# Kernel tuning notes

Measured on AMD Instinct MI355X. Metric: run time of the kernel, lower is better.

The kernel has to match this reference:

```python
import jax, jax.numpy as jnp
import numpy as np

M, K, N, R = 8192, 4096, 4096, 32
GROUP = 64  # nunchaku W4A4 quantization group size
QMAX = 7.0  # int4 symmetric


def setup_inputs() -> dict:
    key = jax.random.key(0)
    ks = jax.random.split(key, 6)
    x = jax.random.normal(ks[0], (M, K), dtype=jnp.float32)
    w_res = jax.random.normal(ks[1], (N, K), dtype=jnp.float32) * 0.02
    lora_down = jax.random.normal(ks[2], (K, R), dtype=jnp.float32) * 0.02
    lora_up = jax.random.normal(ks[3], (N, R), dtype=jnp.float32) * 0.02
    smooth = 0.5 + jax.random.uniform(ks[4], (K,), dtype=jnp.float32)  # positive 1/s factors
    b = jax.random.normal(ks[5], (N,), dtype=jnp.float32)
    return {"x": x, "w_res": w_res, "lora_down": lora_down, "lora_up": lora_up, "smooth": smooth, "b": b}


def _fake_quant_int4(t, group):
    # symmetric int4 fake-quant with per-group absmax scales along last dim
    shp = t.shape
    tg = t.reshape(shp[:-1] + (shp[-1] // group, group))
    scale = jnp.maximum(jnp.max(jnp.abs(tg), axis=-1, keepdims=True) / QMAX, 1e-8)
    q = jnp.clip(jnp.round(tg / scale), -8.0, 7.0) * scale
    return q.reshape(shp)


def reference(x, w_res, lora_down, lora_up, smooth, b):
    # smoothed activation (smooth = 1/s applied by kernel before quantization)
    xs = x * smooth[None, :]                       # [M, K]
    xq = _fake_quant_int4(xs, GROUP)               # per-token per-group int4
    wq = _fake_quant_int4(w_res, GROUP)            # per-outchannel per-group int4
    # W4A4 GEMM on dequantized values + fused low-rank LoRA correction + bias
    main = jnp.einsum('mk,nk->mn', xq, wq)         # [M, N]
    lora = jnp.einsum('mr,nr->mn', xs @ lora_down, lora_up)
    return main + lora + b[None, :]
```

## Files before the change

kernel.cpp:

```cpp
#include <hip/hip_runtime.h>
#include <hip/hip_bf16.h>
#include <stdint.h>

#define M_DIM 8192
#define N_DIM 4096
#define K_DIM 4096
#define R_DIM 32
#define KPAD  4160
#define NT    65
#define QMAXF 7.0f

using bf16_t = __hip_bfloat16;
typedef __attribute__((ext_vector_type(4))) float f32x4;
typedef __attribute__((ext_vector_type(8))) short bf16x8;

__device__ __forceinline__ void stage16(const void* g, void* l) {
#if defined(__has_builtin) && __has_builtin(__builtin_amdgcn_global_load_lds)
  __builtin_amdgcn_global_load_lds(
      (const __attribute__((address_space(1))) unsigned int*)g,
      (__attribute__((address_space(3))) unsigned int*)l, 16, 0, 0);
#else
  *(uint4*)l = *(const uint4*)g;
#endif
}

__global__ __launch_bounds__(256) void prep_kernel(
    const float* __restrict__ x, const float* __restrict__ smooth,
    const float* __restrict__ w, const float* __restrict__ lora_up,
    const float* __restrict__ ld,
    bf16_t* __restrict__ Ap, bf16_t* __restrict__ Bp,
    bf16_t* __restrict__ ldT) {
  const int bid = blockIdx.x;
  const int tid = threadIdx.x;

  if (bid < M_DIM) {
    const int row = bid;
    const int k0  = tid * 16;
    const float* xr = x + (size_t)row * K_DIM + k0;
    const float* sr = smooth + k0;

    float v[16];
#pragma unroll
    for (int i = 0; i < 4; ++i) {
      float4 xv = *(const float4*)(xr + i * 4);
      float4 sv = *(const float4*)(sr + i * 4);
      v[i*4+0] = xv.x * sv.x; v[i*4+1] = xv.y * sv.y;
      v[i*4+2] = xv.z * sv.z; v[i*4+3] = xv.w * sv.w;
    }
    float am = 0.f;
#pragma unroll
    for (int i = 0; i < 16; ++i) am = fmaxf(am, fabsf(v[i]));
    am = fmaxf(am, __shfl_xor(am, 1));
    am = fmaxf(am, __shfl_xor(am, 2));
    const float scale = fmaxf(am / QMAXF, 1e-8f);

    alignas(16) bf16_t o[16];
#pragma unroll
    for (int i = 0; i < 16; ++i) {
      float q = rintf(v[i] / scale);
      q = fminf(fmaxf(q, -8.f), 7.f);
      o[i] = __float2bfloat16(q * scale);
    }
    bf16_t* dst = Ap + (size_t)row * KPAD + k0;
    ((uint4*)dst)[0] = ((uint4*)o)[0];
    ((uint4*)dst)[1] = ((uint4*)o)[1];
    if (tid < 32) Ap[(size_t)row * KPAD + 4128 + tid] = __float2bfloat16(0.f);

  } else if (bid < M_DIM + N_DIM) {
    const int row = bid - M_DIM;
    const int k0  = tid * 16;
    const float* wr = w + (size_t)row * K_DIM + k0;

    float v[16];
#pragma unroll
    for (int i = 0; i < 4; ++i) {
      float4 wv = *(const float4*)(wr + i * 4);
      v[i*4+0] = wv.x; v[i*4+1] = wv.y; v[i*4+2] = wv.z; v[i*4+3] = wv.w;
    }
    float am = 0.f;
#pragma unroll
    for (int i = 0; i < 16; ++i) am = fmaxf(am, fabsf(v[i]));
    am = fmaxf(am, __shfl_xor(am, 1));
    am = fmaxf(am, __shfl_xor(am, 2));
    const float scale = fmaxf(am / QMAXF, 1e-8f);

    alignas(16) bf16_t o[16];
#pragma unroll
    for (int i = 0; i < 16; ++i) {
      float q = rintf(v[i] / scale);
      q = fminf(fmaxf(q, -8.f), 7.f);
      o[i] = __float2bfloat16(q * scale);
    }
    bf16_t* dst = Bp + (size_t)row * KPAD + k0;
    ((uint4*)dst)[0] = ((uint4*)o)[0];
    ((uint4*)dst)[1] = ((uint4*)o)[1];
    if (tid < 32) {
      Bp[(size_t)row * KPAD + 4096 + tid] = __float2bfloat16(lora_up[row * R_DIM + tid]);
    } else if (tid < 64) {
      Bp[(size_t)row * KPAD + 4096 + tid] = __float2bfloat16(0.f);
    }

  } else {
    const int k = (bid - M_DIM - N_DIM) * 256 + tid;
    float v[R_DIM];
#pragma unroll
    for (int i = 0; i < R_DIM / 4; ++i) {
      float4 a = *(const float4*)(ld + (size_t)k * R_DIM + i * 4);
      v[i*4+0] = a.x; v[i*4+1] = a.y; v[i*4+2] = a.z; v[i*4+3] = a.w;
    }
#pragma unroll
    for (int r = 0; r < R_DIM; ++r)
      ldT[(size_t)r * K_DIM + k] = __float2bfloat16(v[r]);
  }
}

__global__ __launch_bounds__(256) void lora_mfma_kernel(
    const float* __restrict__ x, const float* __restrict__ smooth,
    const bf16_t* __restrict__ ldT, bf16_t* __restrict__ Ap) {
  const int tid  = threadIdx.x;
  const int w    = tid >> 6;
  const int lane = tid & 63;
  const int m0   = blockIdx.x * 32;

  const int mrow = m0 + (w >> 1) * 16 + (lane & 15);
  const int ncol = (w & 1) * 16 + (lane & 15);
  const float* xr = x + (size_t)mrow * K_DIM;
  const bf16_t* br = ldT + (size_t)ncol * K_DIM;

  f32x4 acc = {0.f, 0.f, 0.f, 0.f};
  union { bf16_t h[8]; bf16x8 v; } au;

  for (int k = 0; k < K_DIM; k += 32) {
    const int kf = k + (lane >> 4) * 8;
    float4 x0 = *(const float4*)(xr + kf);
    float4 x1 = *(const float4*)(xr + kf + 4);
    float4 s0 = *(const float4*)(smooth + kf);
    float4 s1 = *(const float4*)(smooth + kf + 4);
    au.h[0] = __float2bfloat16(x0.x * s0.x);
    au.h[1] = __float2bfloat16(x0.y * s0.y);
    au.h[2] = __float2bfloat16(x0.z * s0.z);
    au.h[3] = __float2bfloat16(x0.w * s0.w);
    au.h[4] = __float2bfloat16(x1.x * s1.x);
    au.h[5] = __float2bfloat16(x1.y * s1.y);
    au.h[6] = __float2bfloat16(x1.z * s1.z);
    au.h[7] = __float2bfloat16(x1.w * s1.w);
    bf16x8 bv = *(const bf16x8*)(br + kf);
    acc = __builtin_amdgcn_mfma_f32_16x16x32_bf16(au.v, bv, acc, 0, 0, 0);
  }

  const int orow = m0 + (w >> 1) * 16 + (lane >> 4) * 4;
  const int ocol = 4096 + ncol;
#pragma unroll
  for (int q = 0; q < 4; ++q)
    Ap[(size_t)(orow + q) * KPAD + ocol] = __float2bfloat16(acc[q]);
}

__global__ __launch_bounds__(512, 2) void gemm_kernel(
    const bf16_t* __restrict__ A, const bf16_t* __restrict__ B,
    const float* __restrict__ bias, float* __restrict__ C) {
  extern __shared__ __align__(16) bf16_t lds[];

  const int wg  = blockIdx.x;
  const int swz = (wg & 7) * 64 + (wg >> 3);
  const int bn  = swz & 15;
  const int bm  = swz >> 4;

  const int tid  = threadIdx.x;
  const int lane = tid & 63;
  const int wid  = tid >> 6;
  const int wm   = wid >> 2;
  const int wn   = wid & 3;

  const int lr = lane & 15;
  const int lg = lane >> 4;
  const int l7 = lane & 7;
  const int gk0 = ((0 + lg) ^ l7) * 8;
  const int gk1 = ((4 + lg) ^ l7) * 8;

  const int sr   = tid >> 3;
  const int sl   = tid & 7;
  const int gcol = (sl ^ (sr & 7)) * 8;
  const bf16_t* Abase = A + (size_t)(bm * 256 + ((sr >> 5) & 1) * 128 + (sr & 31)) * KPAD + gcol;
  const bf16_t* Bbase = B + (size_t)(bn * 256 + sr) * KPAD + gcol;
  bf16_t* ldsb = lds;

#define STAGE_A(buf, h, kt) do {                                               \
    stage16(Abase + (size_t)((h) * 2 + 0) * 32 * KPAD + (kt) * 64,             \
            ldsb + (buf) * 32768 + (h) * 8192 + 0 * 4096 + tid * 8);           \
    stage16(Abase + (size_t)((h) * 2 + 1) * 32 * KPAD + (kt) * 64,             \
            ldsb + (buf) * 32768 + (h) * 8192 + 1 * 4096 + tid * 8);           \
  } while (0)
#define STAGE_B(buf, h, kt) do {                                               \
    stage16(Bbase + (size_t)((h) * 128 + 0) * KPAD + (kt) * 64,                \
            ldsb + (buf) * 32768 + 16384 + (h) * 8192 + 0 * 4096 + tid * 8);   \
    stage16(Bbase + (size_t)((h) * 128 + 64) * KPAD + (kt) * 64,               \
            ldsb + (buf) * 32768 + 16384 + (h) * 8192 + 1 * 4096 + tid * 8);   \
  } while (0)

  f32x4  acc[8][4] = {};
  bf16x8 aA[2][2];
  bf16x8 aB[2][2];
  bf16x8 bF[4][2];

#define LOAD_A(DST, q, cb) do {                                                \
    const bf16_t* pa_ = ldsb + (cb) * 32768 + ((q) * 64 + wm * 32 + lr) * 64;  \
    DST[0][0] = *(const bf16x8*)(pa_ + gk0);                                   \
    DST[0][1] = *(const bf16x8*)(pa_ + gk1);                                   \
    DST[1][0] = *(const bf16x8*)(pa_ + 1024 + gk0);                            \
    DST[1][1] = *(const bf16x8*)(pa_ + 1024 + gk1);                            \
  } while (0)
#define LOAD_BN(nbuf) do {                                                     \
    _Pragma("unroll")                                                          \
    for (int j = 0; j < 4; ++j) {                                              \
      const bf16_t* pb_ = ldsb + (nbuf) * 32768 + 16384 + (wn * 64 + j * 16 + lr) * 64; \
      bF[j][0] = *(const bf16x8*)(pb_ + gk0);                                  \
      bF[j][1] = *(const bf16x8*)(pb_ + gk1);                                  \
    }                                                                          \
  } while (0)
#define MFMA_Q(q, AARR) do {                                                   \
    _Pragma("unroll")                                                          \
    for (int i = 0; i < 2; ++i)                                                \
      _Pragma("unroll")                                                        \
      for (int j = 0; j < 4; ++j) {                                            \
        acc[(q)*2+i][j] = __builtin_amdgcn_mfma_f32_16x16x32_bf16(             \
            AARR[i][0], bF[j][0], acc[(q)*2+i][j], 0, 0, 0);                   \
        acc[(q)*2+i][j] = __builtin_amdgcn_mfma_f32_16x16x32_bf16(             \
            AARR[i][1], bF[j][1], acc[(q)*2+i][j], 0, 0, 0);                   \
      }                                                                        \
  } while (0)

#define KTILE(u, cur) do {                                                     \
                                                             \
    if ((u) + 1 < NT) STAGE_A((cur) ^ 1, 1, (u) + 1);                          \
    __builtin_amdgcn_s_barrier();                                              \
    asm volatile("s_waitcnt lgkmcnt(0)" ::: "memory");                         \
    __builtin_amdgcn_sched_barrier(0);                                         \
    LOAD_A(aB, 1, cur);                                                        \
    __builtin_amdgcn_sched_barrier(0);                                         \
    __builtin_amdgcn_s_setprio(1);                                             \
    MFMA_Q(0, aA);                                                             \
    __builtin_amdgcn_s_setprio(0);                                             \
    __builtin_amdgcn_s_barrier();                                              \
                                                             \
    if ((u) + 2 < NT) STAGE_B(cur, 0, (u) + 2);                                \
    __builtin_amdgcn_s_barrier();                                              \
    asm volatile("s_waitcnt lgkmcnt(0)" ::: "memory");                         \
    __builtin_amdgcn_sched_barrier(0);                                         \
    LOAD_A(aA, 2, cur);                                                        \
    __builtin_amdgcn_sched_barrier(0);                                         \
    __builtin_amdgcn_s_setprio(1);                                             \
    MFMA_Q(1, aB);                                                             \
    __builtin_amdgcn_s_setprio(0);                                             \
    __builtin_amdgcn_s_barrier();                                              \
                                                             \
    if ((u) + 2 < NT) STAGE_B(cur, 1, (u) + 2);                                \
    __builtin_amdgcn_s_barrier();                                              \
    asm volatile("s_waitcnt lgkmcnt(0)" ::: "memory");                         \
    __builtin_amdgcn_sched_barrier(0);                                         \
    LOAD_A(aB, 3, cur);                                                        \
    __builtin_amdgcn_sched_barrier(0);                                         \
    __builtin_amdgcn_s_setprio(1);                                             \
    MFMA_Q(2, aA);                                                             \
    __builtin_amdgcn_s_setprio(0);                                             \
    __builtin_amdgcn_s_barrier();                                              \
                                                             \
    if ((u) + 2 < NT) {                                                        \
      STAGE_A(cur, 0, (u) + 2);                                                \
      asm volatile("s_waitcnt vmcnt(6)" ::: "memory");                         \
    } else {                                                                   \
      asm volatile("s_waitcnt vmcnt(0)" ::: "memory");                         \
    }                                                                          \
    __builtin_amdgcn_s_barrier();                                              \
    asm volatile("s_waitcnt lgkmcnt(0)" ::: "memory");                         \
    __builtin_amdgcn_sched_barrier(0);                                         \
    if ((u) + 1 < NT) LOAD_A(aA, 0, (cur) ^ 1);                                \
    __builtin_amdgcn_sched_barrier(0);                                         \
    __builtin_amdgcn_s_setprio(1);                                             \
    MFMA_Q(3, aB);                                                             \
    __builtin_amdgcn_s_setprio(0);                                             \
    __builtin_amdgcn_sched_barrier(0);                                         \
    if ((u) + 1 < NT) LOAD_BN((cur) ^ 1);                                      \
    __builtin_amdgcn_s_barrier();                                              \
  } while (0)

  STAGE_B(0, 0, 0); STAGE_B(0, 1, 0); STAGE_A(0, 0, 0); STAGE_A(0, 1, 0);
  STAGE_B(1, 0, 1); STAGE_B(1, 1, 1); STAGE_A(1, 0, 1);
  asm volatile("s_waitcnt vmcnt(6)" ::: "memory");
  __builtin_amdgcn_s_barrier();
  LOAD_BN(0);
  LOAD_A(aA, 0, 0);

  for (int base = 0; base < 64; base += 2) {
    KTILE(base,     0);
    KTILE(base + 1, 1);
  }
  KTILE(64, 0);

  const int colb = bn * 256 + wn * 64 + lr;
  const int rowb = bm * 256 + wm * 128 + lg * 4;
#pragma unroll
  for (int j = 0; j < 4; ++j) {
    const int gc = colb + j * 16;
    const float bv = bias[gc];
#pragma unroll
    for (int q = 0; q < 4; ++q)
#pragma unroll
      for (int i = 0; i < 2; ++i) {
        const int gr = rowb + q * 32 + i * 16;
#pragma unroll
        for (int e = 0; e < 4; ++e)
          C[(size_t)(gr + e) * N_DIM + gc] = acc[q * 2 + i][j][e] + bv;
      }
  }
#undef STAGE_A
#undef STAGE_B
#undef LOAD_A
#undef LOAD_BN
#undef MFMA_Q
#undef KTILE
}

extern "C" void kernel_launch(void* const* d_in, const int* in_sizes, int n_in,
                              void* d_out, int out_size, void* d_ws, size_t ws_size,
                              hipStream_t stream) {
  const float* x         = (const float*)d_in[0];
  const float* w_res     = (const float*)d_in[1];
  const float* lora_down = (const float*)d_in[2];
  const float* lora_up   = (const float*)d_in[3];
  const float* smooth    = (const float*)d_in[4];
  const float* b         = (const float*)d_in[5];
  float* out = (float*)d_out;

  bf16_t* Ap  = (bf16_t*)d_ws;
  bf16_t* Bp  = Ap + (size_t)M_DIM * KPAD;
  bf16_t* ldT = Bp + (size_t)N_DIM * KPAD;

  hipFuncSetAttribute((const void*)gemm_kernel,
                      hipFuncAttributeMaxDynamicSharedMemorySize, 131072);

  prep_kernel<<<M_DIM + N_DIM + K_DIM / 256, 256, 0, stream>>>(
      x, smooth, w_res, lora_up, lora_down, Ap, Bp, ldT);
  lora_mfma_kernel<<<M_DIM / 32, 256, 0, stream>>>(x, smooth, ldT, Ap);
  gemm_kernel<<<(M_DIM / 256) * (N_DIM / 256), 512, 131072, stream>>>(Ap, Bp, b, out);
}
```

Before: 358.2 us.

## Switch GEMM to 32x32x16 MFMA with two-phase k-tile schedule

Replaces the 16x16x32 bf16 MFMA tiling with 32x32x16 MFMA instructions and f32x16 accumulators, so each wave issues fewer, larger matrix ops and does fewer LDS fragment loads per flop. The k-tile loop is restructured from four sub-phases into two halves, with all B-tile staging moved into the second half and the prefetch of next-tile fragments removed. This cuts barrier count but loses LDS-load/MFMA overlap across tiles and may raise register pressure.

```diff
diff --git a/kernel.cpp b/kernel.cpp
--- a/kernel.cpp
+++ b/kernel.cpp
@@ -11,8 +11,9 @@
 #define QMAXF 7.0f
 
 using bf16_t = __hip_bfloat16;
-typedef __attribute__((ext_vector_type(4))) float f32x4;
-typedef __attribute__((ext_vector_type(8))) short bf16x8;
+typedef __attribute__((ext_vector_type(4)))  float f32x4;
+typedef __attribute__((ext_vector_type(16))) float f32x16;
+typedef __attribute__((ext_vector_type(8)))  short bf16x8;
 
 __device__ __forceinline__ void stage16(const void* g, void* l) {
 #if defined(__has_builtin) && __has_builtin(__builtin_amdgcn_global_load_lds)
@@ -171,11 +172,9 @@
   const int wm   = wid >> 2;
   const int wn   = wid & 3;
 
-  const int lr = lane & 15;
-  const int lg = lane >> 4;
-  const int l7 = lane & 7;
-  const int gk0 = ((0 + lg) ^ l7) * 8;
-  const int gk1 = ((4 + lg) ^ l7) * 8;
+  const int l31 = lane & 31;
+  const int lh  = lane >> 5;
+  const int l7  = lane & 7;
 
   const int sr   = tid >> 3;
   const int sl   = tid & 7;
@@ -197,74 +196,57 @@
             ldsb + (buf) * 32768 + 16384 + (h) * 8192 + 1 * 4096 + tid * 8);   \
   } while (0)
 
-  f32x4  acc[8][4] = {};
-  bf16x8 aA[2][2];
-  bf16x8 aB[2][2];
-  bf16x8 bF[4][2];
-
-#define LOAD_A(DST, q, cb) do {                                                \
-    const bf16_t* pa_ = ldsb + (cb) * 32768 + ((q) * 64 + wm * 32 + lr) * 64;  \
-    DST[0][0] = *(const bf16x8*)(pa_ + gk0);                                   \
-    DST[0][1] = *(const bf16x8*)(pa_ + gk1);                                   \
-    DST[1][0] = *(const bf16x8*)(pa_ + 1024 + gk0);                            \
-    DST[1][1] = *(const bf16x8*)(pa_ + 1024 + gk1);                            \
-  } while (0)
-#define LOAD_BN(nbuf) do {                                                     \
+  f32x16 acc[8] = {};
+  bf16x8 aF[2][4];
+  bf16x8 bF[2][4];
+
+#define RCOL(kt) ((((kt) * 2 + lh) ^ l7) * 8)
+
+#define LOAD_B_ALL(cb) do {                                                    \
     _Pragma("unroll")                                                          \
-    for (int j = 0; j < 4; ++j) {                                              \
-      const bf16_t* pb_ = ldsb + (nbuf) * 32768 + 16384 + (wn * 64 + j * 16 + lr) * 64; \
-      bF[j][0] = *(const bf16x8*)(pb_ + gk0);                                  \
-      bF[j][1] = *(const bf16x8*)(pb_ + gk1);                                  \
+    for (int ct = 0; ct < 2; ++ct) {                                           \
+      const bf16_t* pb_ = ldsb + (cb) * 32768 + 16384 +                        \
+                          (wn * 64 + ct * 32 + l31) * 64;                      \
+      _Pragma("unroll")                                                        \
+      for (int kt = 0; kt < 4; ++kt) bF[ct][kt] = *(const bf16x8*)(pb_ + RCOL(kt)); \
     }                                                                          \
   } while (0)
-#define MFMA_Q(q, AARR) do {                                                   \
+#define LOAD_A_HALF(h, cb) do {                                                \
     _Pragma("unroll")                                                          \
-    for (int i = 0; i < 2; ++i)                                                \
+    for (int i = 0; i < 2; ++i) {                                              \
+      const bf16_t* pa_ = ldsb + (cb) * 32768 +                                \
+                          (((h) * 2 + i) * 64 + wm * 32 + l31) * 64;           \
       _Pragma("unroll")                                                        \
-      for (int j = 0; j < 4; ++j) {                                            \
-        acc[(q)*2+i][j] = __builtin_amdgcn_mfma_f32_16x16x32_bf16(             \
-            AARR[i][0], bF[j][0], acc[(q)*2+i][j], 0, 0, 0);                   \
-        acc[(q)*2+i][j] = __builtin_amdgcn_mfma_f32_16x16x32_bf16(             \
-            AARR[i][1], bF[j][1], acc[(q)*2+i][j], 0, 0, 0);                   \
-      }                                                                        \
-  } while (0)
-
-#define KTILE(u, cur) do {                                                     \
-                                                             \
+      for (int kt = 0; kt < 4; ++kt) aF[i][kt] = *(const bf16x8*)(pa_ + RCOL(kt)); \
+    }                                                                          \
+  } while (0)
+#define MFMA_HALF(h) do {                                                      \
+    _Pragma("unroll")                                                          \
+    for (int kt = 0; kt < 4; ++kt)                                             \
+      _Pragma("unroll")                                                        \
+      for (int i = 0; i < 2; ++i)                                              \
+        _Pragma("unroll")                                                      \
+        for (int ct = 0; ct < 2; ++ct)                                         \
+          acc[((h)*2+i)*2+ct] = __builtin_amdgcn_mfma_f32_32x32x16_bf16(       \
+              aF[i][kt], bF[ct][kt], acc[((h)*2+i)*2+ct], 0, 0, 0);            \
+  } while (0)
+
+#define KTILE2(u, cur) do {                                                    \
+                           \
+    LOAD_B_ALL(cur);                                                           \
+    LOAD_A_HALF(0, cur);                                                       \
     if ((u) + 1 < NT) STAGE_A((cur) ^ 1, 1, (u) + 1);                          \
     __builtin_amdgcn_s_barrier();                                              \
     asm volatile("s_waitcnt lgkmcnt(0)" ::: "memory");                         \
-    __builtin_amdgcn_sched_barrier(0);                                         \
-    LOAD_A(aB, 1, cur);                                                        \
-    __builtin_amdgcn_sched_barrier(0);                                         \
     __builtin_amdgcn_s_setprio(1);                                             \
-    MFMA_Q(0, aA);                                                             \
+    MFMA_HALF(0);                                                              \
     __builtin_amdgcn_s_setprio(0);                                             \
     __builtin_amdgcn_s_barrier();                                              \
-                                                             \
-    if ((u) + 2 < NT) STAGE_B(cur, 0, (u) + 2);                                \
-    __builtin_amdgcn_s_barrier();                                              \
-    asm volatile("s_waitcnt lgkmcnt(0)" ::: "memory");                         \
-    __builtin_amdgcn_sched_barrier(0);                                         \
-    LOAD_A(aA, 2, cur);                                                        \
-    __builtin_amdgcn_sched_barrier(0);                                         \
-    __builtin_amdgcn_s_setprio(1);                                             \
-    MFMA_Q(1, aB);                                                             \
-    __builtin_amdgcn_s_setprio(0);                                             \
-    __builtin_amdgcn_s_barrier();                                              \
-                                                             \
-    if ((u) + 2 < NT) STAGE_B(cur, 1, (u) + 2);                                \
-    __builtin_amdgcn_s_barrier();                                              \
-    asm volatile("s_waitcnt lgkmcnt(0)" ::: "memory");                         \
-    __builtin_amdgcn_sched_barrier(0);                                         \
-    LOAD_A(aB, 3, cur);                                                        \
-    __builtin_amdgcn_sched_barrier(0);                                         \
-    __builtin_amdgcn_s_setprio(1);                                             \
-    MFMA_Q(2, aA);                                                             \
-    __builtin_amdgcn_s_setprio(0);                                             \
-    __builtin_amdgcn_s_barrier();                                              \
-                                                             \
+              \
+    LOAD_A_HALF(1, cur);                                                       \
     if ((u) + 2 < NT) {                                                        \
+      STAGE_B(cur, 0, (u) + 2);                                                \
+      STAGE_B(cur, 1, (u) + 2);                                                \
       STAGE_A(cur, 0, (u) + 2);                                                \
       asm volatile("s_waitcnt vmcnt(6)" ::: "memory");                         \
     } else {                                                                   \
@@ -272,14 +254,9 @@
     }                                                                          \
     __builtin_amdgcn_s_barrier();                                              \
     asm volatile("s_waitcnt lgkmcnt(0)" ::: "memory");                         \
-    __builtin_amdgcn_sched_barrier(0);                                         \
-    if ((u) + 1 < NT) LOAD_A(aA, 0, (cur) ^ 1);                                \
-    __builtin_amdgcn_sched_barrier(0);                                         \
     __builtin_amdgcn_s_setprio(1);                                             \
-    MFMA_Q(3, aB);                                                             \
+    MFMA_HALF(1);                                                              \
     __builtin_amdgcn_s_setprio(0);                                             \
-    __builtin_amdgcn_sched_barrier(0);                                         \
-    if ((u) + 1 < NT) LOAD_BN((cur) ^ 1);                                      \
     __builtin_amdgcn_s_barrier();                                              \
   } while (0)
 
@@ -287,37 +264,34 @@
   STAGE_B(1, 0, 1); STAGE_B(1, 1, 1); STAGE_A(1, 0, 1);
   asm volatile("s_waitcnt vmcnt(6)" ::: "memory");
   __builtin_amdgcn_s_barrier();
-  LOAD_BN(0);
-  LOAD_A(aA, 0, 0);
 
   for (int base = 0; base < 64; base += 2) {
-    KTILE(base,     0);
-    KTILE(base + 1, 1);
+    KTILE2(base,     0);
+    KTILE2(base + 1, 1);
   }
-  KTILE(64, 0);
-
-  const int colb = bn * 256 + wn * 64 + lr;
-  const int rowb = bm * 256 + wm * 128 + lg * 4;
-#pragma unroll
-  for (int j = 0; j < 4; ++j) {
-    const int gc = colb + j * 16;
-    const float bv = bias[gc];
-#pragma unroll
-    for (int q = 0; q < 4; ++q)
-#pragma unroll
-      for (int i = 0; i < 2; ++i) {
-        const int gr = rowb + q * 32 + i * 16;
-#pragma unroll
-        for (int e = 0; e < 4; ++e)
-          C[(size_t)(gr + e) * N_DIM + gc] = acc[q * 2 + i][j][e] + bv;
+  KTILE2(64, 0);
+
+#pragma unroll
+  for (int rt = 0; rt < 4; ++rt) {
+#pragma unroll
+    for (int ct = 0; ct < 2; ++ct) {
+      const int gc = bn * 256 + wn * 64 + ct * 32 + l31;
+      const float bv = bias[gc];
+      const int gr0 = bm * 256 + wm * 128 + rt * 32 + lh * 4;
+#pragma unroll
+      for (int e = 0; e < 16; ++e) {
+        const int gr = gr0 + (e & 3) + 8 * (e >> 2);
+        C[(size_t)gr * N_DIM + gc] = acc[rt * 2 + ct][e] + bv;
       }
+    }
   }
 #undef STAGE_A
 #undef STAGE_B
-#undef LOAD_A
-#undef LOAD_BN
-#undef MFMA_Q
-#undef KTILE
+#undef RCOL
+#undef LOAD_B_ALL
+#undef LOAD_A_HALF
+#undef MFMA_HALF
+#undef KTILE2
 }
 
 extern "C" void kernel_launch(void* const* d_in, const int* in_sizes, int n_in,
```

New measurement: 387.6 us. 1.08x slower.

## Fuse activation quantization with LoRA down-projection to read x once

Applied to the files above, without the earlier changes.

Activation smoothing, int4 fake-quantization and the LoRA down-projection MFMA are merged into one kernel. Each block handles 16 rows, with the four waves splitting K and reducing partial LoRA sums through shared memory. The weight prep kernel now processes only the weight and lora_down tensors. This removes the second full read of the fp32 x matrix (128 MB), at the cost of fewer blocks (512) and a per-row K-split that may limit memory parallelism.

```diff
diff --git a/kernel.cpp b/kernel.cpp
--- a/kernel.cpp
+++ b/kernel.cpp
@@ -24,50 +24,15 @@
 #endif
 }
 
-__global__ __launch_bounds__(256) void prep_kernel(
-    const float* __restrict__ x, const float* __restrict__ smooth,
+__global__ __launch_bounds__(256) void prep_w_kernel(
     const float* __restrict__ w, const float* __restrict__ lora_up,
     const float* __restrict__ ld,
-    bf16_t* __restrict__ Ap, bf16_t* __restrict__ Bp,
-    bf16_t* __restrict__ ldT) {
+    bf16_t* __restrict__ Bp, bf16_t* __restrict__ ldT) {
   const int bid = blockIdx.x;
   const int tid = threadIdx.x;
 
-  if (bid < M_DIM) {
+  if (bid < N_DIM) {
     const int row = bid;
-    const int k0  = tid * 16;
-    const float* xr = x + (size_t)row * K_DIM + k0;
-    const float* sr = smooth + k0;
-
-    float v[16];
-#pragma unroll
-    for (int i = 0; i < 4; ++i) {
-      float4 xv = *(const float4*)(xr + i * 4);
-      float4 sv = *(const float4*)(sr + i * 4);
-      v[i*4+0] = xv.x * sv.x; v[i*4+1] = xv.y * sv.y;
-      v[i*4+2] = xv.z * sv.z; v[i*4+3] = xv.w * sv.w;
-    }
-    float am = 0.f;
-#pragma unroll
-    for (int i = 0; i < 16; ++i) am = fmaxf(am, fabsf(v[i]));
-    am = fmaxf(am, __shfl_xor(am, 1));
-    am = fmaxf(am, __shfl_xor(am, 2));
-    const float scale = fmaxf(am / QMAXF, 1e-8f);
-
-    alignas(16) bf16_t o[16];
-#pragma unroll
-    for (int i = 0; i < 16; ++i) {
-      float q = rintf(v[i] / scale);
-      q = fminf(fmaxf(q, -8.f), 7.f);
-      o[i] = __float2bfloat16(q * scale);
-    }
-    bf16_t* dst = Ap + (size_t)row * KPAD + k0;
-    ((uint4*)dst)[0] = ((uint4*)o)[0];
-    ((uint4*)dst)[1] = ((uint4*)o)[1];
-    if (tid < 32) Ap[(size_t)row * KPAD + 4128 + tid] = __float2bfloat16(0.f);
-
-  } else if (bid < M_DIM + N_DIM) {
-    const int row = bid - M_DIM;
     const int k0  = tid * 16;
     const float* wr = w + (size_t)row * K_DIM + k0;
 
@@ -101,7 +66,7 @@
     }
 
   } else {
-    const int k = (bid - M_DIM - N_DIM) * 256 + tid;
+    const int k = (bid - N_DIM) * 256 + tid;
     float v[R_DIM];
 #pragma unroll
     for (int i = 0; i < R_DIM / 4; ++i) {
@@ -114,45 +79,102 @@
   }
 }
 
-__global__ __launch_bounds__(256) void lora_mfma_kernel(
+__global__ __launch_bounds__(256) void fused_x_kernel(
     const float* __restrict__ x, const float* __restrict__ smooth,
     const bf16_t* __restrict__ ldT, bf16_t* __restrict__ Ap) {
+  __shared__ float tpart[3][16][32];
+
   const int tid  = threadIdx.x;
   const int w    = tid >> 6;
   const int lane = tid & 63;
-  const int m0   = blockIdx.x * 32;
-
-  const int mrow = m0 + (w >> 1) * 16 + (lane & 15);
-  const int ncol = (w & 1) * 16 + (lane & 15);
-  const float* xr = x + (size_t)mrow * K_DIM;
-  const bf16_t* br = ldT + (size_t)ncol * K_DIM;
-
-  f32x4 acc = {0.f, 0.f, 0.f, 0.f};
-  union { bf16_t h[8]; bf16x8 v; } au;
-
-  for (int k = 0; k < K_DIM; k += 32) {
-    const int kf = k + (lane >> 4) * 8;
-    float4 x0 = *(const float4*)(xr + kf);
-    float4 x1 = *(const float4*)(xr + kf + 4);
-    float4 s0 = *(const float4*)(smooth + kf);
-    float4 s1 = *(const float4*)(smooth + kf + 4);
-    au.h[0] = __float2bfloat16(x0.x * s0.x);
-    au.h[1] = __float2bfloat16(x0.y * s0.y);
-    au.h[2] = __float2bfloat16(x0.z * s0.z);
-    au.h[3] = __float2bfloat16(x0.w * s0.w);
-    au.h[4] = __float2bfloat16(x1.x * s1.x);
-    au.h[5] = __float2bfloat16(x1.y * s1.y);
-    au.h[6] = __float2bfloat16(x1.z * s1.z);
-    au.h[7] = __float2bfloat16(x1.w * s1.w);
-    bf16x8 bv = *(const bf16x8*)(br + kf);
-    acc = __builtin_amdgcn_mfma_f32_16x16x32_bf16(au.v, bv, acc, 0, 0, 0);
-  }
-
-  const int orow = m0 + (w >> 1) * 16 + (lane >> 4) * 4;
-  const int ocol = 4096 + ncol;
-#pragma unroll
-  for (int q = 0; q < 4; ++q)
-    Ap[(size_t)(orow + q) * KPAD + ocol] = __float2bfloat16(acc[q]);
+  const int r    = lane & 15;
+  const int kg   = lane >> 4;
+  const int m0   = blockIdx.x * 16;
+  const int mrow = m0 + r;
+
+  const float*  xr  = x + (size_t)mrow * K_DIM;
+  const bf16_t* br0 = ldT + (size_t)r * K_DIM;
+  const bf16_t* br1 = ldT + (size_t)(16 + r) * K_DIM;
+
+  f32x4 acc0 = {0.f, 0.f, 0.f, 0.f};
+  f32x4 acc1 = {0.f, 0.f, 0.f, 0.f};
+  const int kbase = w * 1024;
+
+  for (int s = 0; s < 32; s += 2) {
+    const int ke = kbase + s * 32 + kg * 8;
+    const int ko = ke + 32;
+
+    float v[16];
+    union { bf16_t h[8]; bf16x8 vv; } aue, auo;
+    {
+      float4 x0 = *(const float4*)(xr + ke);
+      float4 x1 = *(const float4*)(xr + ke + 4);
+      float4 s0 = *(const float4*)(smooth + ke);
+      float4 s1 = *(const float4*)(smooth + ke + 4);
+      v[0] = x0.x * s0.x; v[1] = x0.y * s0.y; v[2] = x0.z * s0.z; v[3] = x0.w * s0.w;
+      v[4] = x1.x * s1.x; v[5] = x1.y * s1.y; v[6] = x1.z * s1.z; v[7] = x1.w * s1.w;
+    }
+    {
+      float4 x0 = *(const float4*)(xr + ko);
+      float4 x1 = *(const float4*)(xr + ko + 4);
+      float4 s0 = *(const float4*)(smooth + ko);
+      float4 s1 = *(const float4*)(smooth + ko + 4);
+      v[8]  = x0.x * s0.x; v[9]  = x0.y * s0.y; v[10] = x0.z * s0.z; v[11] = x0.w * s0.w;
+      v[12] = x1.x * s1.x; v[13] = x1.y * s1.y; v[14] = x1.z * s1.z; v[15] = x1.w * s1.w;
+    }
+#pragma unroll
+    for (int i = 0; i < 8; ++i) {
+      aue.h[i] = __float2bfloat16(v[i]);
+      auo.h[i] = __float2bfloat16(v[8 + i]);
+    }
+
+    acc0 = __builtin_amdgcn_mfma_f32_16x16x32_bf16(aue.vv, *(const bf16x8*)(br0 + ke), acc0, 0, 0, 0);
+    acc1 = __builtin_amdgcn_mfma_f32_16x16x32_bf16(aue.vv, *(const bf16x8*)(br1 + ke), acc1, 0, 0, 0);
+    acc0 = __builtin_amdgcn_mfma_f32_16x16x32_bf16(auo.vv, *(const bf16x8*)(br0 + ko), acc0, 0, 0, 0);
+    acc1 = __builtin_amdgcn_mfma_f32_16x16x32_bf16(auo.vv, *(const bf16x8*)(br1 + ko), acc1, 0, 0, 0);
+
+    float am = 0.f;
+#pragma unroll
+    for (int i = 0; i < 16; ++i) am = fmaxf(am, fabsf(v[i]));
+    am = fmaxf(am, __shfl_xor(am, 16));
+    am = fmaxf(am, __shfl_xor(am, 32));
+    const float scale = fmaxf(am / QMAXF, 1e-8f);
+
+    alignas(16) bf16_t o[16];
+#pragma unroll
+    for (int i = 0; i < 16; ++i) {
+      float q = rintf(v[i] / scale);
+      q = fminf(fmaxf(q, -8.f), 7.f);
+      o[i] = __float2bfloat16(q * scale);
+    }
+    *(uint4*)(Ap + (size_t)mrow * KPAD + ke) = ((const uint4*)o)[0];
+    *(uint4*)(Ap + (size_t)mrow * KPAD + ko) = ((const uint4*)o)[1];
+  }
+
+  if (w != 0) {
+#pragma unroll
+    for (int q = 0; q < 4; ++q) {
+      tpart[w - 1][kg * 4 + q][r]      = acc0[q];
+      tpart[w - 1][kg * 4 + q][16 + r] = acc1[q];
+    }
+  }
+  __syncthreads();
+  if (w == 0) {
+#pragma unroll
+    for (int q = 0; q < 4; ++q) {
+      const int orow = m0 + kg * 4 + q;
+      float s0 = acc0[q], s1 = acc1[q];
+#pragma unroll
+      for (int j = 0; j < 3; ++j) {
+        s0 += tpart[j][kg * 4 + q][r];
+        s1 += tpart[j][kg * 4 + q][16 + r];
+      }
+      Ap[(size_t)orow * KPAD + 4096 + r]      = __float2bfloat16(s0);
+      Ap[(size_t)orow * KPAD + 4096 + 16 + r] = __float2bfloat16(s1);
+    }
+    alignas(16) bf16_t z[8] = {};
+    *(uint4*)(Ap + (size_t)mrow * KPAD + 4128 + kg * 8) = *(const uint4*)z;
+  }
 }
 
 __global__ __launch_bounds__(512, 2) void gemm_kernel(
@@ -338,8 +360,8 @@
   hipFuncSetAttribute((const void*)gemm_kernel,
                       hipFuncAttributeMaxDynamicSharedMemorySize, 131072);
 
-  prep_kernel<<<M_DIM + N_DIM + K_DIM / 256, 256, 0, stream>>>(
-      x, smooth, w_res, lora_up, lora_down, Ap, Bp, ldT);
-  lora_mfma_kernel<<<M_DIM / 32, 256, 0, stream>>>(x, smooth, ldT, Ap);
+  prep_w_kernel<<<N_DIM + K_DIM / 256, 256, 0, stream>>>(
+      w_res, lora_up, lora_down, Bp, ldT);
+  fused_x_kernel<<<M_DIM / 16, 256, 0, stream>>>(x, smooth, ldT, Ap);
   gemm_kernel<<<(M_DIM / 256) * (N_DIM / 256), 512, 131072, stream>>>(Ap, Bp, b, out);
 }
```

New measurement: 302.8 us. 15.5% less time.
